# Kernel tuning notes

Hardware: AMD Instinct MI355X
Metric: run time of the kernel (lower is better)

Reference implementation:

```python
import jax, jax.numpy as jnp
import numpy as np

N_NODES = 100000


def setup_inputs() -> dict:
    key = jax.random.key(0)
    k1, k2, k3, k4, k5 = jax.random.split(key, 5)
    features = jax.random.normal(k1, (N_NODES, 512), dtype=jnp.float32)
    edge_src = jax.random.randint(k2, (640000,), 0, N_NODES, dtype=jnp.int64)
    edge_dst = jax.random.randint(k3, (640000,), 0, N_NODES, dtype=jnp.int64)
    edge_weight = jax.random.uniform(k4, (640000,), dtype=jnp.float32)
    weights = jax.random.normal(k5, (512, 128), dtype=jnp.float32) * (2.0 / 512) ** 0.5  # kaiming-ish scale
    bias = jnp.zeros((128,), dtype=jnp.float32)
    return {
        "features": features,
        "edge_src": edge_src,
        "edge_dst": edge_dst,
        "edge_weight": edge_weight,
        "weights": weights,
        "bias": bias,
    }


def reference(features, edge_src, edge_dst, edge_weight, weights, bias):
    # X' = A @ (X @ W) + b, with sparse A given as COO edges (src -> dst).
    h = jnp.matmul(features, weights)                      # [N, d_out] dense GEMM
    msg = edge_weight[:, None] * h[edge_src]               # [E, d_out] gather + scale
    out = jax.ops.segment_sum(msg, edge_dst, num_segments=N_NODES)  # sparse aggregation
    return out + bias
```

## Files before the change

### kernel.cpp

```cpp
#include <hip/hip_runtime.h>


#define D_IN  512
#define D_OUT 128

typedef __attribute__((ext_vector_type(8))) short short8;
typedef __attribute__((ext_vector_type(4))) float f32x4;
typedef __attribute__((ext_vector_type(4))) int i32x4;
typedef __attribute__((ext_vector_type(8))) unsigned short u16x8;

typedef __attribute__((address_space(1))) const unsigned int glob_u32;
typedef __attribute__((address_space(3))) unsigned int lds_u32;

static __device__ __forceinline__ unsigned short f2bf(float f) {
    unsigned u = __float_as_uint(f);
    unsigned r = (u + 0x7FFFu + ((u >> 16) & 1u)) >> 16;
    return (unsigned short)r;
}

static __device__ __forceinline__ int pack2(float lo, float hi) {
    return (int)((__float_as_uint(hi) & 0xFFFF0000u) | (__float_as_uint(lo) >> 16));
}

__global__ __launch_bounds__(256) void prep_kernel(const float* __restrict__ W,
                                                   unsigned short* __restrict__ Wt,
                                                   int* __restrict__ deg, int M) {
    int t = blockIdx.x * 256 + threadIdx.x;
    if (t < D_OUT * D_IN) {
        int n = t >> 9;
        int k = t & 511;
        Wt[t] = f2bf(W[(size_t)k * D_OUT + n]);
    }
    if (t < M) deg[t] = 0;
}

__global__ __launch_bounds__(256, 3) void gemm_kernel(const float* __restrict__ X,
                                                      const unsigned short* __restrict__ Wt,
                                                      unsigned short* __restrict__ H, int M) {
    __shared__ float As[128 * 64];
    __shared__ unsigned short Bs[128 * 64];

    const int tid = threadIdx.x;
    const int lane = tid & 63;
    const int w = tid >> 6;
    const int block_row = blockIdx.x * 128;

    const int m = lane & 15;
    const int q = lane >> 4;
    const int wave_row = (w >> 1) * 64;
    const int wave_col = (w & 1) * 64;

    f32x4 acc[4][4];
#pragma unroll
    for (int a = 0; a < 4; a++)
#pragma unroll
        for (int b = 0; b < 4; b++) acc[a][b] = (f32x4){0.f, 0.f, 0.f, 0.f};

    for (int kc = 0; kc < D_IN; kc += 64) {
#pragma unroll
        for (int it = 0; it < 8; it++) {
            int slot_base = w * 512 + it * 64;
            int s = slot_base + lane;
            int row = s >> 4;
            int kq = (s & 15) ^ (row & 15);
            int grow = block_row + row;
            if (grow >= M) grow = M - 1;
            const float* gp = X + (size_t)grow * D_IN + kc + kq * 4;
            __builtin_amdgcn_global_load_lds((glob_u32*)gp,
                                             (lds_u32*)(As + (size_t)slot_base * 4),
                                             16, 0, 0);
        }
#pragma unroll
        for (int it = 0; it < 4; it++) {
            int slot_base = w * 256 + it * 64;
            int s = slot_base + lane;
            int n = s >> 3;
            int kq8 = (s & 7) ^ (n & 7);
            const unsigned short* gp = Wt + (size_t)n * D_IN + kc + kq8 * 8;
            __builtin_amdgcn_global_load_lds((glob_u32*)gp,
                                             (lds_u32*)(Bs + (size_t)slot_base * 8),
                                             16, 0, 0);
        }
        __syncthreads();

#pragma unroll
        for (int ks = 0; ks < 2; ks++) {
            const int ksub = ks * 32;
            short8 afr[4];
#pragma unroll
            for (int rg = 0; rg < 4; rg++) {
                int row = wave_row + rg * 16 + m;
                int kq0 = (ksub >> 2) + 2 * q;
                float4 u0 = *reinterpret_cast<const float4*>(
                    As + (size_t)(row * 16 + (kq0 ^ (row & 15))) * 4);
                float4 u1 = *reinterpret_cast<const float4*>(
                    As + (size_t)(row * 16 + ((kq0 + 1) ^ (row & 15))) * 4);
                i32x4 ai;
                ai.x = pack2(u0.x, u0.y);
                ai.y = pack2(u0.z, u0.w);
                ai.z = pack2(u1.x, u1.y);
                ai.w = pack2(u1.z, u1.w);
                afr[rg] = __builtin_bit_cast(short8, ai);
            }
            short8 bfr[4];
#pragma unroll
            for (int cg = 0; cg < 4; cg++) {
                int n = wave_col + cg * 16 + m;
                int kq8 = (ksub >> 3) + q;
                bfr[cg] = *reinterpret_cast<const short8*>(
                    Bs + (size_t)(n * 8 + (kq8 ^ (n & 7))) * 8);
            }
#pragma unroll
            for (int rg = 0; rg < 4; rg++)
#pragma unroll
                for (int cg = 0; cg < 4; cg++)
                    acc[rg][cg] = __builtin_amdgcn_mfma_f32_16x16x32_bf16(
                        afr[rg], bfr[cg], acc[rg][cg], 0, 0, 0);
        }
        __syncthreads();
    }

#pragma unroll
    for (int rg = 0; rg < 4; rg++) {
#pragma unroll
        for (int r = 0; r < 4; r++) {
            int grow = block_row + wave_row + rg * 16 + q * 4 + r;
            if (grow < M) {
#pragma unroll
                for (int cg = 0; cg < 4; cg++)
                    H[(size_t)grow * D_OUT + wave_col + cg * 16 + m] = f2bf(acc[rg][cg][r]);
            }
        }
    }
}

__global__ __launch_bounds__(256) void hist_kernel(const int* __restrict__ dst,
                                                   int* __restrict__ deg, int E) {
    int e = blockIdx.x * 256 + threadIdx.x;
    if (e < E) atomicAdd(&deg[dst[e]], 1);
}

__global__ __launch_bounds__(256) void scan1_kernel(const int* __restrict__ deg,
                                                    int* __restrict__ rs,
                                                    int* __restrict__ bsum, int M) {
    __shared__ int sdata[256];
    const int tid = threadIdx.x;
    const int base = blockIdx.x * 1024 + tid * 4;
    int v[4];
#pragma unroll
    for (int i = 0; i < 4; i++) v[i] = (base + i < M) ? deg[base + i] : 0;
    int tsum = v[0] + v[1] + v[2] + v[3];
    sdata[tid] = tsum;
    __syncthreads();
    for (int off = 1; off < 256; off <<= 1) {
        int add = (tid >= off) ? sdata[tid - off] : 0;
        __syncthreads();
        sdata[tid] += add;
        __syncthreads();
    }
    int excl = sdata[tid] - tsum;
#pragma unroll
    for (int i = 0; i < 4; i++) {
        if (base + i < M) rs[base + i] = excl;
        excl += v[i];
    }
    if (tid == 255) bsum[blockIdx.x] = sdata[255];
}

__global__ __launch_bounds__(128) void scan2_kernel(int* __restrict__ bsum, int NB) {
    __shared__ int sdata[128];
    const int tid = threadIdx.x;
    int v = (tid < NB) ? bsum[tid] : 0;
    sdata[tid] = v;
    __syncthreads();
    for (int off = 1; off < 128; off <<= 1) {
        int add = (tid >= off) ? sdata[tid - off] : 0;
        __syncthreads();
        sdata[tid] += add;
        __syncthreads();
    }
    if (tid < NB) bsum[tid] = sdata[tid] - v;
}

__global__ __launch_bounds__(256) void scan3_kernel(int* __restrict__ rs,
                                                    int* __restrict__ cur,
                                                    const int* __restrict__ bsum,
                                                    int M, int E) {
    int i = blockIdx.x * 256 + threadIdx.x;
    if (i < M) {
        int val = rs[i] + bsum[i >> 10];
        rs[i] = val;
        cur[i] = val;
    }
    if (i == 0) rs[M] = E;
}

__global__ __launch_bounds__(256) void build_kernel(const int* __restrict__ src,
                                                    const int* __restrict__ dst,
                                                    const float* __restrict__ w,
                                                    int* __restrict__ cur,
                                                    unsigned long long* __restrict__ csr,
                                                    int E) {
    int e = blockIdx.x * 256 + threadIdx.x;
    if (e >= E) return;
    int d = dst[e];
    int pos = atomicAdd(&cur[d], 1);
    csr[pos] = ((unsigned long long)__float_as_uint(w[e]) << 32) | (unsigned)src[e];
}

__global__ __launch_bounds__(256) void agg_kernel(const unsigned short* __restrict__ H,
                                                  const int* __restrict__ rs,
                                                  const unsigned long long* __restrict__ csr,
                                                  const float* __restrict__ bias,
                                                  float* __restrict__ out, int M) {
    int row = blockIdx.x * 16 + (threadIdx.x >> 4);
    if (row >= M) return;
    int sub = threadIdx.x & 15;

    float acc[8];
#pragma unroll
    for (int c = 0; c < 8; c++) acc[c] = bias[sub * 8 + c];

    int j = rs[row];
    int end = rs[row + 1];

    for (; j + 4 <= end; j += 4) {
        unsigned long long p0 = csr[j];
        unsigned long long p1 = csr[j + 1];
        unsigned long long p2 = csr[j + 2];
        unsigned long long p3 = csr[j + 3];
        u16x8 v0 = *reinterpret_cast<const u16x8*>(
            H + (size_t)(unsigned)(p0 & 0xFFFFFFFFull) * D_OUT + sub * 8);
        u16x8 v1 = *reinterpret_cast<const u16x8*>(
            H + (size_t)(unsigned)(p1 & 0xFFFFFFFFull) * D_OUT + sub * 8);
        u16x8 v2 = *reinterpret_cast<const u16x8*>(
            H + (size_t)(unsigned)(p2 & 0xFFFFFFFFull) * D_OUT + sub * 8);
        u16x8 v3 = *reinterpret_cast<const u16x8*>(
            H + (size_t)(unsigned)(p3 & 0xFFFFFFFFull) * D_OUT + sub * 8);
        float w0 = __uint_as_float((unsigned)(p0 >> 32));
        float w1 = __uint_as_float((unsigned)(p1 >> 32));
        float w2 = __uint_as_float((unsigned)(p2 >> 32));
        float w3 = __uint_as_float((unsigned)(p3 >> 32));
#pragma unroll
        for (int c = 0; c < 8; c++) {
            acc[c] += w0 * __uint_as_float((unsigned)v0[c] << 16);
            acc[c] += w1 * __uint_as_float((unsigned)v1[c] << 16);
            acc[c] += w2 * __uint_as_float((unsigned)v2[c] << 16);
            acc[c] += w3 * __uint_as_float((unsigned)v3[c] << 16);
        }
    }
    for (; j < end; j++) {
        unsigned long long p0 = csr[j];
        float w0 = __uint_as_float((unsigned)(p0 >> 32));
        u16x8 v0 = *reinterpret_cast<const u16x8*>(
            H + (size_t)(unsigned)(p0 & 0xFFFFFFFFull) * D_OUT + sub * 8);
#pragma unroll
        for (int c = 0; c < 8; c++)
            acc[c] += w0 * __uint_as_float((unsigned)v0[c] << 16);
    }

    float4 o0 = make_float4(acc[0], acc[1], acc[2], acc[3]);
    float4 o1 = make_float4(acc[4], acc[5], acc[6], acc[7]);
    *reinterpret_cast<float4*>(out + (size_t)row * D_OUT + sub * 8) = o0;
    *reinterpret_cast<float4*>(out + (size_t)row * D_OUT + sub * 8 + 4) = o1;
}

extern "C" void kernel_launch(void* const* d_in, const int* in_sizes, int n_in,
                              void* d_out, int out_size, void* d_ws, size_t ws_size,
                              hipStream_t stream) {
    const float* features    = (const float*)d_in[0];
    const int*   edge_src    = (const int*)d_in[1];
    const int*   edge_dst    = (const int*)d_in[2];
    const float* edge_weight = (const float*)d_in[3];
    const float* weights     = (const float*)d_in[4];
    const float* bias        = (const float*)d_in[5];
    float* out = (float*)d_out;

    const int M = in_sizes[0] / D_IN;
    const int E = in_sizes[1];

    char* ws = (char*)d_ws;
    unsigned short* hbf = (unsigned short*)(ws);
    unsigned short* Wt  = (unsigned short*)(ws + 25600000);
    int* deg            = (int*)(ws + 25731072);
    int* rs             = (int*)(ws + 26131072);
    int* cur            = (int*)(ws + 26531088);
    unsigned long long* csr = (unsigned long long*)(ws + 26931088);
    int* bsum           = (int*)(ws + 32051088);

    prep_kernel<<<(M + 255) / 256, 256, 0, stream>>>(weights, Wt, deg, M);
    gemm_kernel<<<(M + 127) / 128, 256, 0, stream>>>(features, Wt, hbf, M);
    hist_kernel<<<(E + 255) / 256, 256, 0, stream>>>(edge_dst, deg, E);
    const int NB = (M + 1023) / 1024;
    scan1_kernel<<<NB, 256, 0, stream>>>(deg, rs, bsum, M);
    scan2_kernel<<<1, 128, 0, stream>>>(bsum, NB);
    scan3_kernel<<<(M + 255) / 256, 256, 0, stream>>>(rs, cur, bsum, M, E);
    build_kernel<<<(E + 255) / 256, 256, 0, stream>>>(edge_src, edge_dst, edge_weight,
                                                      cur, csr, E);
    agg_kernel<<<(M + 15) / 16, 256, 0, stream>>>(hbf, rs, csr, bias, out, M);
}
```

Measured before the change: 415.4 us.

## Double-buffer GEMM K-chunks with smaller tile and use wave-per-row aggregation

The GEMM now processes 64-row tiles and prefetches the next K-chunk of X and W into a second LDS buffer while computing on the current one, overlapping global-to-LDS loads with MFMA work. Occupancy hint drops to 2 blocks per CU because LDS usage grows, and W is reloaded twice as often across blocks. The aggregation kernel assigns a full 64-lane wave per destination row, each lane gathering one 32-bit pair of bf16 values, trading wider vector loads for more parallel rows in flight and simpler per-thread arithmetic.

```diff
diff --git a/kernel.cpp b/kernel.cpp
--- a/kernel.cpp
+++ b/kernel.cpp
@@ -7,7 +7,6 @@
 typedef __attribute__((ext_vector_type(8))) short short8;
 typedef __attribute__((ext_vector_type(4))) float f32x4;
 typedef __attribute__((ext_vector_type(4))) int i32x4;
-typedef __attribute__((ext_vector_type(8))) unsigned short u16x8;
 
 typedef __attribute__((address_space(1))) const unsigned int glob_u32;
 typedef __attribute__((address_space(3))) unsigned int lds_u32;
@@ -34,67 +33,74 @@
     if (t < M) deg[t] = 0;
 }
 
-__global__ __launch_bounds__(256, 3) void gemm_kernel(const float* __restrict__ X,
+__global__ __launch_bounds__(256, 2) void gemm_kernel(const float* __restrict__ X,
                                                       const unsigned short* __restrict__ Wt,
                                                       unsigned short* __restrict__ H, int M) {
-    __shared__ float As[128 * 64];
-    __shared__ unsigned short Bs[128 * 64];
+    __shared__ float As[2][64 * 64];
+    __shared__ unsigned short Bs[2][128 * 64];
 
     const int tid = threadIdx.x;
     const int lane = tid & 63;
     const int w = tid >> 6;
-    const int block_row = blockIdx.x * 128;
+    const int block_row = blockIdx.x * 64;
 
     const int m = lane & 15;
     const int q = lane >> 4;
-    const int wave_row = (w >> 1) * 64;
+    const int wave_row = (w >> 1) * 32;
     const int wave_col = (w & 1) * 64;
 
-    f32x4 acc[4][4];
-#pragma unroll
-    for (int a = 0; a < 4; a++)
+    f32x4 acc[2][4];
+#pragma unroll
+    for (int a = 0; a < 2; a++)
 #pragma unroll
         for (int b = 0; b < 4; b++) acc[a][b] = (f32x4){0.f, 0.f, 0.f, 0.f};
 
-    for (int kc = 0; kc < D_IN; kc += 64) {
-#pragma unroll
-        for (int it = 0; it < 8; it++) {
-            int slot_base = w * 512 + it * 64;
-            int s = slot_base + lane;
-            int row = s >> 4;
-            int kq = (s & 15) ^ (row & 15);
-            int grow = block_row + row;
-            if (grow >= M) grow = M - 1;
-            const float* gp = X + (size_t)grow * D_IN + kc + kq * 4;
-            __builtin_amdgcn_global_load_lds((glob_u32*)gp,
-                                             (lds_u32*)(As + (size_t)slot_base * 4),
-                                             16, 0, 0);
-        }
-#pragma unroll
-        for (int it = 0; it < 4; it++) {
-            int slot_base = w * 256 + it * 64;
-            int s = slot_base + lane;
-            int n = s >> 3;
-            int kq8 = (s & 7) ^ (n & 7);
-            const unsigned short* gp = Wt + (size_t)n * D_IN + kc + kq8 * 8;
-            __builtin_amdgcn_global_load_lds((glob_u32*)gp,
-                                             (lds_u32*)(Bs + (size_t)slot_base * 8),
-                                             16, 0, 0);
-        }
-        __syncthreads();
+#define STAGE_CHUNK(KC, BUF)                                                          \
+    {                                                                                 \
+        _Pragma("unroll")                                                             \
+        for (int it = 0; it < 4; it++) {                                              \
+            int slot_base = w * 256 + it * 64;                                        \
+            int s = slot_base + lane;                                                 \
+            int row = s >> 4;                                                         \
+            int kq = (s & 15) ^ (row & 15);                                           \
+            int grow = block_row + row;                                               \
+            if (grow >= M) grow = M - 1;                                              \
+            const float* gp = X + (size_t)grow * D_IN + (KC) + kq * 4;                \
+            __builtin_amdgcn_global_load_lds((glob_u32*)gp,                           \
+                (lds_u32*)(&As[BUF][0] + (size_t)slot_base * 4), 16, 0, 0);           \
+        }                                                                             \
+        _Pragma("unroll")                                                             \
+        for (int it = 0; it < 4; it++) {                                              \
+            int slot_base = w * 256 + it * 64;                                        \
+            int s = slot_base + lane;                                                 \
+            int n = s >> 3;                                                           \
+            int kq8 = (s & 7) ^ (n & 7);                                              \
+            const unsigned short* gp = Wt + (size_t)n * D_IN + (KC) + kq8 * 8;        \
+            __builtin_amdgcn_global_load_lds((glob_u32*)gp,                           \
+                (lds_u32*)(&Bs[BUF][0] + (size_t)slot_base * 8), 16, 0, 0);           \
+        }                                                                             \
+    }
+
+    STAGE_CHUNK(0, 0);
+    __syncthreads();
+
+#pragma unroll
+    for (int c = 0; c < 8; c++) {
+        const int cur = c & 1;
+        if (c < 7) STAGE_CHUNK((c + 1) * 64, cur ^ 1);
 
 #pragma unroll
         for (int ks = 0; ks < 2; ks++) {
             const int ksub = ks * 32;
-            short8 afr[4];
-#pragma unroll
-            for (int rg = 0; rg < 4; rg++) {
+            short8 afr[2];
+#pragma unroll
+            for (int rg = 0; rg < 2; rg++) {
                 int row = wave_row + rg * 16 + m;
                 int kq0 = (ksub >> 2) + 2 * q;
                 float4 u0 = *reinterpret_cast<const float4*>(
-                    As + (size_t)(row * 16 + (kq0 ^ (row & 15))) * 4);
+                    &As[cur][0] + (size_t)(row * 16 + (kq0 ^ (row & 15))) * 4);
                 float4 u1 = *reinterpret_cast<const float4*>(
-                    As + (size_t)(row * 16 + ((kq0 + 1) ^ (row & 15))) * 4);
+                    &As[cur][0] + (size_t)(row * 16 + ((kq0 + 1) ^ (row & 15))) * 4);
                 i32x4 ai;
                 ai.x = pack2(u0.x, u0.y);
                 ai.y = pack2(u0.z, u0.w);
@@ -108,10 +114,10 @@
                 int n = wave_col + cg * 16 + m;
                 int kq8 = (ksub >> 3) + q;
                 bfr[cg] = *reinterpret_cast<const short8*>(
-                    Bs + (size_t)(n * 8 + (kq8 ^ (n & 7))) * 8);
+                    &Bs[cur][0] + (size_t)(n * 8 + (kq8 ^ (n & 7))) * 8);
             }
 #pragma unroll
-            for (int rg = 0; rg < 4; rg++)
+            for (int rg = 0; rg < 2; rg++)
 #pragma unroll
                 for (int cg = 0; cg < 4; cg++)
                     acc[rg][cg] = __builtin_amdgcn_mfma_f32_16x16x32_bf16(
@@ -121,7 +127,7 @@
     }
 
 #pragma unroll
-    for (int rg = 0; rg < 4; rg++) {
+    for (int rg = 0; rg < 2; rg++) {
 #pragma unroll
         for (int r = 0; r < 4; r++) {
             int grow = block_row + wave_row + rg * 16 + q * 4 + r;
@@ -132,6 +138,7 @@
             }
         }
     }
+#undef STAGE_CHUNK
 }
 
 __global__ __launch_bounds__(256) void hist_kernel(const int* __restrict__ dst,
@@ -213,56 +220,46 @@
                                                   const unsigned long long* __restrict__ csr,
                                                   const float* __restrict__ bias,
                                                   float* __restrict__ out, int M) {
-    int row = blockIdx.x * 16 + (threadIdx.x >> 4);
+    int row = blockIdx.x * 4 + (threadIdx.x >> 6);
     if (row >= M) return;
-    int sub = threadIdx.x & 15;
-
-    float acc[8];
-#pragma unroll
-    for (int c = 0; c < 8; c++) acc[c] = bias[sub * 8 + c];
-
+    int c = threadIdx.x & 63;
+
+    float2 acc = *((const float2*)bias + c);
     int j = rs[row];
     int end = rs[row + 1];
+    const unsigned int* Hc = (const unsigned int*)H + c;
 
     for (; j + 4 <= end; j += 4) {
         unsigned long long p0 = csr[j];
         unsigned long long p1 = csr[j + 1];
         unsigned long long p2 = csr[j + 2];
         unsigned long long p3 = csr[j + 3];
-        u16x8 v0 = *reinterpret_cast<const u16x8*>(
-            H + (size_t)(unsigned)(p0 & 0xFFFFFFFFull) * D_OUT + sub * 8);
-        u16x8 v1 = *reinterpret_cast<const u16x8*>(
-            H + (size_t)(unsigned)(p1 & 0xFFFFFFFFull) * D_OUT + sub * 8);
-        u16x8 v2 = *reinterpret_cast<const u16x8*>(
-            H + (size_t)(unsigned)(p2 & 0xFFFFFFFFull) * D_OUT + sub * 8);
-        u16x8 v3 = *reinterpret_cast<const u16x8*>(
-            H + (size_t)(unsigned)(p3 & 0xFFFFFFFFull) * D_OUT + sub * 8);
+        unsigned v0 = Hc[(size_t)(unsigned)(p0 & 0xFFFFFFFFull) * 64];
+        unsigned v1 = Hc[(size_t)(unsigned)(p1 & 0xFFFFFFFFull) * 64];
+        unsigned v2 = Hc[(size_t)(unsigned)(p2 & 0xFFFFFFFFull) * 64];
+        unsigned v3 = Hc[(size_t)(unsigned)(p3 & 0xFFFFFFFFull) * 64];
         float w0 = __uint_as_float((unsigned)(p0 >> 32));
         float w1 = __uint_as_float((unsigned)(p1 >> 32));
         float w2 = __uint_as_float((unsigned)(p2 >> 32));
         float w3 = __uint_as_float((unsigned)(p3 >> 32));
-#pragma unroll
-        for (int c = 0; c < 8; c++) {
-            acc[c] += w0 * __uint_as_float((unsigned)v0[c] << 16);
-            acc[c] += w1 * __uint_as_float((unsigned)v1[c] << 16);
-            acc[c] += w2 * __uint_as_float((unsigned)v2[c] << 16);
-            acc[c] += w3 * __uint_as_float((unsigned)v3[c] << 16);
-        }
+        acc.x += w0 * __uint_as_float(v0 << 16);
+        acc.y += w0 * __uint_as_float(v0 & 0xFFFF0000u);
+        acc.x += w1 * __uint_as_float(v1 << 16);
+        acc.y += w1 * __uint_as_float(v1 & 0xFFFF0000u);
+        acc.x += w2 * __uint_as_float(v2 << 16);
+        acc.y += w2 * __uint_as_float(v2 & 0xFFFF0000u);
+        acc.x += w3 * __uint_as_float(v3 << 16);
+        acc.y += w3 * __uint_as_float(v3 & 0xFFFF0000u);
     }
     for (; j < end; j++) {
         unsigned long long p0 = csr[j];
         float w0 = __uint_as_float((unsigned)(p0 >> 32));
-        u16x8 v0 = *reinterpret_cast<const u16x8*>(
-            H + (size_t)(unsigned)(p0 & 0xFFFFFFFFull) * D_OUT + sub * 8);
-#pragma unroll
-        for (int c = 0; c < 8; c++)
-            acc[c] += w0 * __uint_as_float((unsigned)v0[c] << 16);
-    }
-
-    float4 o0 = make_float4(acc[0], acc[1], acc[2], acc[3]);
-    float4 o1 = make_float4(acc[4], acc[5], acc[6], acc[7]);
-    *reinterpret_cast<float4*>(out + (size_t)row * D_OUT + sub * 8) = o0;
-    *reinterpret_cast<float4*>(out + (size_t)row * D_OUT + sub * 8 + 4) = o1;
+        unsigned v0 = Hc[(size_t)(unsigned)(p0 & 0xFFFFFFFFull) * 64];
+        acc.x += w0 * __uint_as_float(v0 << 16);
+        acc.y += w0 * __uint_as_float(v0 & 0xFFFF0000u);
+    }
+
+    *((float2*)(out + (size_t)row * D_OUT) + c) = acc;
 }
 
 extern "C" void kernel_launch(void* const* d_in, const int* in_sizes, int n_in,
@@ -289,7 +286,7 @@
     int* bsum           = (int*)(ws + 32051088);
 
     prep_kernel<<<(M + 255) / 256, 256, 0, stream>>>(weights, Wt, deg, M);
-    gemm_kernel<<<(M + 127) / 128, 256, 0, stream>>>(features, Wt, hbf, M);
+    gemm_kernel<<<(M + 63) / 64, 256, 0, stream>>>(features, Wt, hbf, M);
     hist_kernel<<<(E + 255) / 256, 256, 0, stream>>>(edge_dst, deg, E);
     const int NB = (M + 1023) / 1024;
     scan1_kernel<<<NB, 256, 0, stream>>>(deg, rs, bsum, M);
@@ -297,5 +294,5 @@
     scan3_kernel<<<(M + 255) / 256, 256, 0, stream>>>(rs, cur, bsum, M, E);
     build_kernel<<<(E + 255) / 256, 256, 0, stream>>>(edge_src, edge_dst, edge_weight,
                                                       cur, csr, E);
-    agg_kernel<<<(M + 15) / 16, 256, 0, stream>>>(hbf, rs, csr, bias, out, M);
-}
+    agg_kernel<<<(M + 3) / 4, 256, 0, stream>>>(hbf, rs, csr, bias, out, M);
+}
```

After: 423.5 us. No clear change (+1.9%).
